# Performance work log

Hardware: AMD Instinct MI355X
Metric: run time of the kernel (lower is better)

The kernel has to match this reference:

```python
import jax, jax.numpy as jnp
import numpy as np

SHAPES = ((64, 64), (32, 32), (16, 16), (8, 8))
LEVEL_STARTS = np.concatenate([[0], np.cumsum([h * w for h, w in SHAPES])]).tolist()
N_LEVELS = 4; N_HEADS = 8; N_POINTS = 4; D_MODEL = 256; HEAD_DIM = 32; D_FFN = 1024; NUM_LAYERS = 2
LEN_IN = sum(h * w for h, w in SHAPES)
BATCH = 2


def setup_inputs():
    key = jax.random.key(0)
    ks = iter(jax.random.split(key, 40))
    r = lambda shape, s=1.0: jax.random.normal(next(ks), shape, dtype=jnp.float32) * s
    L = NUM_LAYERS
    return {
        "src": r((BATCH, LEN_IN, D_MODEL)),
        "pos": r((BATCH, LEN_IN, D_MODEL), 0.5),
        "valid_ratios": jnp.ones((BATCH, N_LEVELS, 2), jnp.float32),
        "Wv": r((L, D_MODEL, D_MODEL), 0.05), "bv": jnp.zeros((L, D_MODEL), jnp.float32),
        "Woff": r((L, D_MODEL, N_HEADS * N_LEVELS * N_POINTS * 2), 0.002),
        "boff": r((L, N_HEADS * N_LEVELS * N_POINTS * 2), 0.5),
        "Wa": r((L, D_MODEL, N_HEADS * N_LEVELS * N_POINTS), 0.05),
        "ba": jnp.zeros((L, N_HEADS * N_LEVELS * N_POINTS), jnp.float32),
        "Wo": r((L, D_MODEL, D_MODEL), 0.05), "bo": jnp.zeros((L, D_MODEL), jnp.float32),
        "g1": jnp.ones((L, D_MODEL), jnp.float32), "be1": jnp.zeros((L, D_MODEL), jnp.float32),
        "Wl1": r((L, D_MODEL, D_FFN), 0.05), "bl1": jnp.zeros((L, D_FFN), jnp.float32),
        "Wl2": r((L, D_FFN, D_MODEL), 0.05), "bl2": jnp.zeros((L, D_MODEL), jnp.float32),
        "g2": jnp.ones((L, D_MODEL), jnp.float32), "be2": jnp.zeros((L, D_MODEL), jnp.float32),
    }


def layer_norm(x, g, b, eps=1e-5):
    m = jnp.mean(x, -1, keepdims=True)
    v = jnp.mean(jnp.square(x - m), -1, keepdims=True)
    return (x - m) * jax.lax.rsqrt(v + eps) * g + b


def make_reference_points(valid_ratios):
    # DeformableTransformerEncoder.get_reference_points, vectorized per level
    refs = []
    for lvl, (H, W) in enumerate(SHAPES):
        gy, gx = jnp.meshgrid(jnp.arange(H, dtype=jnp.float32) + 0.5,
                              jnp.arange(W, dtype=jnp.float32) + 0.5, indexing="ij")
        ry = gy.reshape(-1)[None] / (valid_ratios[:, lvl, 1][:, None] * H)
        rx = gx.reshape(-1)[None] / (valid_ratios[:, lvl, 0][:, None] * W)
        refs.append(jnp.stack([rx, ry], -1))  # [N, H*W, 2]
    ref = jnp.concatenate(refs, 1)  # [N, Len, 2]
    return ref[:, :, None, :] * valid_ratios[:, None]  # [N, Len, n_levels, 2]


def ms_deform_attn(query, input_flatten, reference_points, Wv, bv, Woff, boff, Wa, ba, Wo, bo):
    N, Lq, _ = query.shape
    value = (input_flatten @ Wv + bv).reshape(N, -1, N_HEADS, HEAD_DIM)
    off = (query @ Woff + boff).reshape(N, Lq, N_HEADS, N_LEVELS, N_POINTS, 2)
    aw = (query @ Wa + ba).reshape(N, Lq, N_HEADS, N_LEVELS * N_POINTS)
    aw = jax.nn.softmax(aw, -1).reshape(N, Lq, N_HEADS, N_LEVELS, N_POINTS)
    # normalizer is (W, H) per level, as in MSDeformAttn
    normalizer = jnp.array([[w, h] for h, w in SHAPES], jnp.float32)
    loc = reference_points[:, :, None, :, None, :] + off / normalizer[None, None, None, :, None, :]
    acc = jnp.zeros((N, N_HEADS, Lq, HEAD_DIM), query.dtype)
    for lvl, (H, W) in enumerate(SHAPES):
        s = LEVEL_STARTS[lvl]
        val = value[:, s:s + H * W].transpose(0, 2, 1, 3)  # [N, heads, H*W, hd]
        # grid_sample bilinear, align_corners=False, zero padding
        x = loc[:, :, :, lvl, :, 0] * W - 0.5  # [N, Lq, heads, P]
        y = loc[:, :, :, lvl, :, 1] * H - 0.5
        x0 = jnp.floor(x); y0 = jnp.floor(y)
        wx1 = x - x0; wy1 = y - y0
        ix0 = x0.astype(jnp.int32); iy0 = y0.astype(jnp.int32)

        def corner(ix, iy, w):
            valid = (ix >= 0) & (ix < W) & (iy >= 0) & (iy < H)
            idx = jnp.clip(iy, 0, H - 1) * W + jnp.clip(ix, 0, W - 1)
            idx = idx.transpose(0, 2, 1, 3).reshape(N, N_HEADS, Lq * N_POINTS)
            g = jnp.take_along_axis(val, idx[..., None], axis=2).reshape(N, N_HEADS, Lq, N_POINTS, HEAD_DIM)
            w = jnp.where(valid, w, 0.0).transpose(0, 2, 1, 3)  # [N, heads, Lq, P]
            return g * w[..., None]

        sampled = (corner(ix0, iy0, (1 - wx1) * (1 - wy1))
                   + corner(ix0 + 1, iy0, wx1 * (1 - wy1))
                   + corner(ix0, iy0 + 1, (1 - wx1) * wy1)
                   + corner(ix0 + 1, iy0 + 1, wx1 * wy1))
        acc = acc + (sampled * aw[:, :, :, lvl].transpose(0, 2, 1, 3)[..., None]).sum(3)
    out = acc.transpose(0, 2, 1, 3).reshape(N, Lq, D_MODEL)
    return out @ Wo + bo


def reference(src, pos, valid_ratios, Wv, bv, Woff, boff, Wa, ba, Wo, bo,
              g1, be1, Wl1, bl1, Wl2, bl2, g2, be2):
    ref_pts = make_reference_points(valid_ratios)
    out = src
    for l in range(NUM_LAYERS):
        q = out + pos  # with_pos_embed
        attn = ms_deform_attn(q, out, ref_pts, Wv[l], bv[l], Woff[l], boff[l],
                              Wa[l], ba[l], Wo[l], bo[l])
        out = layer_norm(out + attn, g1[l], be1[l])
        ffn = jax.nn.relu(out @ Wl1[l] + bl1[l]) @ Wl2[l] + bl2[l]
        out = layer_norm(out + ffn, g2[l], be2[l])
    return out
```

## Files before the change

kernel.cpp:

```cpp
#include <hip/hip_runtime.h>
#include <math.h>

#define LEN   5440
#define NB    2
#define MROWS (NB * LEN)
#define DM    256
#define NH    8
#define HD    32
#define NLV   4
#define NPT   4
#define DFFN  1024

typedef __attribute__((ext_vector_type(8))) short bf16x8;
typedef __attribute__((ext_vector_type(4))) short bf16x4;
typedef __attribute__((ext_vector_type(4))) float f32x4;

__device__ __forceinline__ short f2bf(float f) {
    union { float f; unsigned u; } cv; cv.f = f;
    unsigned r = cv.u + 0x7fffu + ((cv.u >> 16) & 1u);
    return (short)(r >> 16);
}
__device__ __forceinline__ float bf2f(short s) {
    union { unsigned u; float f; } cv;
    cv.u = ((unsigned)(unsigned short)s) << 16;
    return cv.f;
}

__global__ __launch_bounds__(256) void transpose_convert_all(
    const float* __restrict__ Wv,  const float* __restrict__ Woff,
    const float* __restrict__ Wa,  const float* __restrict__ Wo,
    const float* __restrict__ Wl1, const float* __restrict__ Wl2,
    short* __restrict__ out)
{
    int bx = blockIdx.x;
    int l  = bx / 736;
    int t  = bx % 736;
    const float* src; int K, N; long doff;
    if      (t < 64)  { src = Wv;   K = 256;  N = 256;  doff = 0;      }
    else if (t < 128) { src = Woff; K = 256;  N = 256;  doff = 65536;  t -= 64;  }
    else if (t < 160) { src = Wa;   K = 256;  N = 128;  doff = 131072; t -= 128; }
    else if (t < 224) { src = Wo;   K = 256;  N = 256;  doff = 163840; t -= 160; }
    else if (t < 480) { src = Wl1;  K = 256;  N = 1024; doff = 229376; t -= 224; }
    else              { src = Wl2;  K = 1024; N = 256;  doff = 491520; t -= 480; }
    src += (long)l * K * N;
    short* dst = out + (long)l * 753664 + doff;

    const int ntx = N / 32;
    const int n0 = (t % ntx) * 32, k0 = (t / ntx) * 32;

    __shared__ short T[32][33];
    const int tid = threadIdx.x;
    {
        const int n = tid & 31, kq = tid >> 5;
        #pragma unroll
        for (int i = 0; i < 4; ++i) {
            int k = kq * 4 + i;
            T[n][k] = f2bf(src[(long)(k0 + k) * N + n0 + n]);
        }
    }
    __syncthreads();
    {
        const int k = tid & 31, nq = tid >> 5;
        #pragma unroll
        for (int i = 0; i < 4; ++i) {
            int n = nq * 4 + i;
            dst[(long)(n0 + n) * K + k0 + k] = T[n][k];
        }
    }
}

__global__ __launch_bounds__(256) void convert_src(
    const float4* __restrict__ s4, const float4* __restrict__ p4,
    bf16x4* __restrict__ curb, bf16x4* __restrict__ qb)
{
    const int i = blockIdx.x * 256 + threadIdx.x;
    float4 s = s4[i], p = p4[i];
    bf16x4 c, q;
    c[0] = f2bf(s.x); c[1] = f2bf(s.y); c[2] = f2bf(s.z); c[3] = f2bf(s.w);
    q[0] = f2bf(s.x + p.x); q[1] = f2bf(s.y + p.y);
    q[2] = f2bf(s.z + p.z); q[3] = f2bf(s.w + p.w);
    curb[i] = c; qb[i] = q;
}

template <int BN, int RELU, int OMODE>
__device__ __forceinline__ void gemm_core128(
    short* As, short* Bs,
    const short* __restrict__ A, const short* __restrict__ Wt,
    const float* __restrict__ bias, float* __restrict__ Cf,
    short* __restrict__ Cb,
    int ldc, int m0, int wrow0, int ccol0, int K)
{
    constexpr int NF = BN / 32;
    constexpr int NBJ = BN / 64;
    const int t    = threadIdx.x;
    const int wave = t >> 6, lane = t & 63;
    const int wm   = (wave & 1) * 64;
    const int wn   = (wave >> 1) * (BN / 2);
    const int lm   = lane & 15;
    const int chkg = lane >> 4;
    const int srow = t >> 2;
    const int sc   = t & 3;

    f32x4 acc[4][NF] = {};
    bf16x8 ar[2], br[NBJ];

    #pragma unroll
    for (int j = 0; j < 2; ++j)
        ar[j] = *(const bf16x8*)(A + (long)(m0 + srow + 64 * j) * K + sc * 8);
    #pragma unroll
    for (int j = 0; j < NBJ; ++j)
        br[j] = *(const bf16x8*)(Wt + (long)(wrow0 + srow + 64 * j) * K + sc * 8);

    for (int k0 = 0; k0 < K; k0 += 32) {
        __syncthreads();
        #pragma unroll
        for (int j = 0; j < 2; ++j)
            *(bf16x8*)(&As[(srow + 64 * j) * 40 + sc * 8]) = ar[j];
        #pragma unroll
        for (int j = 0; j < NBJ; ++j)
            *(bf16x8*)(&Bs[(srow + 64 * j) * 40 + sc * 8]) = br[j];
        __syncthreads();

        if (k0 + 32 < K) {
            #pragma unroll
            for (int j = 0; j < 2; ++j)
                ar[j] = *(const bf16x8*)(A + (long)(m0 + srow + 64 * j) * K + k0 + 32 + sc * 8);
            #pragma unroll
            for (int j = 0; j < NBJ; ++j)
                br[j] = *(const bf16x8*)(Wt + (long)(wrow0 + srow + 64 * j) * K + k0 + 32 + sc * 8);
        }

        bf16x8 af[4], bfv[NF];
        #pragma unroll
        for (int s = 0; s < 4; ++s)
            af[s] = *(const bf16x8*)(&As[(wm + s * 16 + lm) * 40 + chkg * 8]);
        #pragma unroll
        for (int u = 0; u < NF; ++u)
            bfv[u] = *(const bf16x8*)(&Bs[(wn + u * 16 + lm) * 40 + chkg * 8]);
        #pragma unroll
        for (int s = 0; s < 4; ++s)
            #pragma unroll
            for (int u = 0; u < NF; ++u)
                acc[s][u] = __builtin_amdgcn_mfma_f32_16x16x32_bf16(
                    af[s], bfv[u], acc[s][u], 0, 0, 0);
    }

    const int col = lane & 15;
    const int rq  = (lane >> 4) * 4;
    #pragma unroll
    for (int s = 0; s < 4; ++s) {
        #pragma unroll
        for (int u = 0; u < NF; ++u) {
            const int gn = ccol0 + wn + u * 16 + col;
            const float bb = bias[gn];
            #pragma unroll
            for (int r = 0; r < 4; ++r) {
                const int gm = m0 + wm + s * 16 + rq + r;
                float v = acc[s][u][r] + bb;
                if (RELU) v = fmaxf(v, 0.f);
                if (OMODE == 0) {
                    Cf[(long)gm * ldc + gn] = v;
                } else if (OMODE == 1) {
                    Cb[(long)gm * ldc + gn] = f2bf(v);
                } else {
                    const int n   = gm / LEN;
                    const int pix = gm - n * LEN;
                    const int h   = gn >> 5, d = gn & 31;
                    Cb[((long)(n * NH + h) * LEN + pix) * 32 + d] = f2bf(v);
                }
            }
        }
    }
}

template <int BN, int RELU, int OMODE>
__global__ __launch_bounds__(256) void gemm128(
    const short* __restrict__ A, const short* __restrict__ Wt,
    const float* __restrict__ bias, float* Cf, short* Cb, int ldc, int K)
{
    __shared__ __align__(16) short As[128 * 40];
    __shared__ __align__(16) short Bs[BN * 40];
    gemm_core128<BN, RELU, OMODE>(As, Bs, A, Wt, bias, Cf, Cb, ldc,
                                  blockIdx.y * 128, blockIdx.x * BN,
                                  blockIdx.x * BN, K);
}

__global__ __launch_bounds__(256) void gemm_qkv128(
    const short* __restrict__ curb, const short* __restrict__ qb,
    const short* __restrict__ Wt, const float* __restrict__ bv,
    const float* __restrict__ boff, const float* __restrict__ ba,
    short* __restrict__ Vb, float* __restrict__ OFF, float* __restrict__ AW)
{
    __shared__ __align__(16) short As[128 * 40];
    __shared__ __align__(16) short Bs[128 * 40];
    const int n0 = blockIdx.x * 128;
    if (n0 < 256) {
        gemm_core128<128, 0, 2>(As, Bs, curb, Wt, bv, (float*)nullptr, Vb,
                                256, blockIdx.y * 128, n0, n0, 256);
    } else if (n0 < 512) {
        gemm_core128<128, 0, 0>(As, Bs, qb, Wt, boff, OFF, (short*)nullptr,
                                256, blockIdx.y * 128, n0, n0 - 256, 256);
    } else {
        gemm_core128<128, 0, 0>(As, Bs, qb, Wt, ba, AW, (short*)nullptr,
                                128, blockIdx.y * 128, n0, n0 - 512, 256);
    }
}

__global__ __launch_bounds__(256) void gemm_ln(
    const short* __restrict__ A, const short* __restrict__ Wt,
    const float* __restrict__ bias, const float* __restrict__ resid,
    const float* __restrict__ g, const float* __restrict__ be,
    float* __restrict__ outf, short* __restrict__ outb,
    short* __restrict__ outq, const float* __restrict__ pos, int K)
{
    __shared__ __align__(16) short As[32 * 40];
    __shared__ __align__(16) short Bs[256 * 40];
    __shared__ float red[2][32][2];

    const int t    = threadIdx.x;
    const int wave = t >> 6, lane = t & 63;
    const int wm   = (wave & 1) * 16;
    const int wn   = (wave >> 1) * 128;
    const int lm   = lane & 15;
    const int chkg = lane >> 4;
    const int srow = t >> 2;
    const int sc   = t & 3;
    const int m0   = blockIdx.x * 32;
    const bool doA = (t < 128);

    f32x4 acc[8] = {};
    bf16x8 ar, br[4];

    if (doA) ar = *(const bf16x8*)(A + (long)(m0 + srow) * K + sc * 8);
    #pragma unroll
    for (int j = 0; j < 4; ++j)
        br[j] = *(const bf16x8*)(Wt + (long)(srow + 64 * j) * K + sc * 8);

    for (int k0 = 0; k0 < K; k0 += 32) {
        __syncthreads();
        if (doA) *(bf16x8*)(&As[srow * 40 + sc * 8]) = ar;
        #pragma unroll
        for (int j = 0; j < 4; ++j)
            *(bf16x8*)(&Bs[(srow + 64 * j) * 40 + sc * 8]) = br[j];
        __syncthreads();

        if (k0 + 32 < K) {
            if (doA) ar = *(const bf16x8*)(A + (long)(m0 + srow) * K + k0 + 32 + sc * 8);
            #pragma unroll
            for (int j = 0; j < 4; ++j)
                br[j] = *(const bf16x8*)(Wt + (long)(srow + 64 * j) * K + k0 + 32 + sc * 8);
        }

        bf16x8 af = *(const bf16x8*)(&As[(wm + lm) * 40 + chkg * 8]);
        #pragma unroll
        for (int u = 0; u < 8; ++u) {
            bf16x8 bfv = *(const bf16x8*)(&Bs[(wn + u * 16 + lm) * 40 + chkg * 8]);
            acc[u] = __builtin_amdgcn_mfma_f32_16x16x32_bf16(af, bfv, acc[u], 0, 0, 0);
        }
    }

    const int rq = (lane >> 4) * 4;
    #pragma unroll
    for (int u = 0; u < 8; ++u) {
        const int gn = wn + u * 16 + lm;
        const float bb = bias[gn];
        #pragma unroll
        for (int r = 0; r < 4; ++r) {
            const int gm = m0 + wm + rq + r;
            acc[u][r] += bb + resid[(long)gm * DM + gn];
        }
    }

    float rs[4], r2[4];
    #pragma unroll
    for (int r = 0; r < 4; ++r) {
        float s = 0.f, s2 = 0.f;
        #pragma unroll
        for (int u = 0; u < 8; ++u) { const float v = acc[u][r]; s += v; s2 += v * v; }
        rs[r] = s; r2[r] = s2;
    }
    #pragma unroll
    for (int o = 1; o < 16; o <<= 1) {
        #pragma unroll
        for (int r = 0; r < 4; ++r) {
            rs[r] += __shfl_xor(rs[r], o, 64);
            r2[r] += __shfl_xor(r2[r], o, 64);
        }
    }
    if (lm == 0) {
        #pragma unroll
        for (int r = 0; r < 4; ++r) {
            red[wave >> 1][wm + rq + r][0] = rs[r];
            red[wave >> 1][wm + rq + r][1] = r2[r];
        }
    }
    __syncthreads();
    #pragma unroll
    for (int r = 0; r < 4; ++r) {
        const int row = wm + rq + r;
        const float ts = red[0][row][0] + red[1][row][0];
        const float t2 = red[0][row][1] + red[1][row][1];
        const float mean = ts * (1.f / DM);
        const float var  = t2 * (1.f / DM) - mean * mean;
        rs[r] = mean;
        r2[r] = rsqrtf(var + 1e-5f);
    }
    #pragma unroll
    for (int u = 0; u < 8; ++u) {
        const int gn = wn + u * 16 + lm;
        const float gg = g[gn], bbe = be[gn];
        #pragma unroll
        for (int r = 0; r < 4; ++r) {
            const int gm = m0 + wm + rq + r;
            const float o = (acc[u][r] - rs[r]) * r2[r] * gg + bbe;
            outf[(long)gm * DM + gn] = o;
            if (outb) outb[(long)gm * DM + gn] = f2bf(o);
            if (outq) outq[(long)gm * DM + gn] = f2bf(o + pos[(long)gm * DM + gn]);
        }
    }
}

__global__ __launch_bounds__(256) void deform_attn_v3(
    const short* __restrict__ Vb,
    const float* __restrict__ OFF,
    const float* __restrict__ AW,
    const float* __restrict__ vr,
    bf16x4* __restrict__ ATTb)
{
    const int starts[5] = {0, 4096, 5120, 5376, 5440};
    const int dims[4]   = {64, 32, 16, 8};

    const int wave = threadIdx.x >> 6;
    const int lane = threadIdx.x & 63;
    const int h    = lane >> 3;
    const int d4   = lane & 7;

    const int gq = blockIdx.x * 4 + wave;
    const int n  = gq / LEN;
    const int q  = gq % LEN;

    int lq = 3;
    if (q < 4096) lq = 0; else if (q < 5120) lq = 1; else if (q < 5376) lq = 2;
    const int r  = q - starts[lq];
    const int Wq = dims[lq];
    const int gy = r / Wq, gx = r % Wq;
    const float vrxq = vr[(n * NLV + lq) * 2 + 0];
    const float vryq = vr[(n * NLV + lq) * 2 + 1];
    const float rx = (gx + 0.5f) / (vrxq * Wq);
    const float ry = (gy + 0.5f) / (vryq * Wq);

    const long row = (long)n * LEN + q;

    const float* awp = AW + row * 128 + h * 16;
    float a[16];
    float mx = -1e30f;
    #pragma unroll
    for (int i = 0; i < 16; ++i) { a[i] = awp[i]; mx = fmaxf(mx, a[i]); }
    float s = 0.f;
    #pragma unroll
    for (int i = 0; i < 16; ++i) { a[i] = __expf(a[i] - mx); s += a[i]; }
    const float inv = 1.f / s;

    const float* offp = OFF + row * 256 + h * 32;

    float4 acc = {0.f, 0.f, 0.f, 0.f};
    #pragma unroll
    for (int lvl = 0; lvl < NLV; ++lvl) {
        const int Hl = dims[lvl];
        const int Wl = Hl;
        const float fW = (float)Wl;
        const int sb = starts[lvl];
        const float lx = rx * vr[(n * NLV + lvl) * 2 + 0];
        const float ly = ry * vr[(n * NLV + lvl) * 2 + 1];
        const short* vb = Vb + ((long)(n * NH + h) * LEN + sb) * 32 + d4 * 4;
        #pragma unroll
        for (int p = 0; p < NPT; ++p) {
            const float ox = offp[lvl * 8 + p * 2 + 0];
            const float oy = offp[lvl * 8 + p * 2 + 1];
            const float x = fmaf(lx, fW, ox) - 0.5f;
            const float y = fmaf(ly, fW, oy) - 0.5f;
            const float x0f = floorf(x), y0f = floorf(y);
            const int ix0 = (int)x0f, iy0 = (int)y0f;
            const float wx1 = x - x0f, wy1 = y - y0f;
            const float wx0 = 1.f - wx1, wy0 = 1.f - wy1;

            const bool vx0 = (ix0 >= 0)     && (ix0 < Wl);
            const bool vx1 = (ix0 + 1 >= 0) && (ix0 + 1 < Wl);
            const bool vy0 = (iy0 >= 0)     && (iy0 < Hl);
            const bool vy1 = (iy0 + 1 >= 0) && (iy0 + 1 < Hl);
            const int cx0 = min(max(ix0, 0), Wl - 1);
            const int cx1 = min(max(ix0 + 1, 0), Wl - 1);
            const int cy0 = min(max(iy0, 0), Hl - 1);
            const int cy1 = min(max(iy0 + 1, 0), Hl - 1);

            const float w00 = (vx0 && vy0) ? wx0 * wy0 : 0.f;
            const float w10 = (vx1 && vy0) ? wx1 * wy0 : 0.f;
            const float w01 = (vx0 && vy1) ? wx0 * wy1 : 0.f;
            const float w11 = (vx1 && vy1) ? wx1 * wy1 : 0.f;

            const bf16x4 g00 = *(const bf16x4*)(vb + (long)(cy0 * Wl + cx0) * 32);
            const bf16x4 g10 = *(const bf16x4*)(vb + (long)(cy0 * Wl + cx1) * 32);
            const bf16x4 g01 = *(const bf16x4*)(vb + (long)(cy1 * Wl + cx0) * 32);
            const bf16x4 g11 = *(const bf16x4*)(vb + (long)(cy1 * Wl + cx1) * 32);

            const float awv = a[lvl * 4 + p] * inv;
            #pragma unroll
            for (int e = 0; e < 4; ++e) {
                float sv = w00 * bf2f(g00[e]) + w10 * bf2f(g10[e])
                         + w01 * bf2f(g01[e]) + w11 * bf2f(g11[e]);
                (&acc.x)[e] += awv * sv;
            }
        }
    }
    bf16x4 ob;
    ob[0] = f2bf(acc.x); ob[1] = f2bf(acc.y);
    ob[2] = f2bf(acc.z); ob[3] = f2bf(acc.w);
    ATTb[row * 64 + h * 8 + d4] = ob;
}

extern "C" void kernel_launch(void* const* d_in, const int* in_sizes, int n_in,
                              void* d_out, int out_size, void* d_ws, size_t ws_size,
                              hipStream_t stream)
{
    const float* src = (const float*)d_in[0];
    const float* pos = (const float*)d_in[1];
    const float* vr  = (const float*)d_in[2];
    const float* Wv_   = (const float*)d_in[3];
    const float* bv_   = (const float*)d_in[4];
    const float* Woff_ = (const float*)d_in[5];
    const float* boff_ = (const float*)d_in[6];
    const float* Wa_   = (const float*)d_in[7];
    const float* ba_   = (const float*)d_in[8];
    const float* Wo_   = (const float*)d_in[9];
    const float* bo_   = (const float*)d_in[10];
    const float* g1_   = (const float*)d_in[11];
    const float* be1_  = (const float*)d_in[12];
    const float* Wl1_  = (const float*)d_in[13];
    const float* bl1_  = (const float*)d_in[14];
    const float* Wl2_  = (const float*)d_in[15];
    const float* bl2_  = (const float*)d_in[16];
    const float* g2_   = (const float*)d_in[17];
    const float* be2_  = (const float*)d_in[18];

    const long SZ = (long)MROWS * DM;
    float* ws = (float*)d_ws;
    float* OFF  = ws;
    float* AW   = OFF + SZ;
    float* XA   = AW  + (long)MROWS * 128;
    float* XB   = XA  + SZ;
    short* Vb   = (short*)(XB + SZ);
    short* curb = Vb   + SZ;
    short* qb   = curb + SZ;
    short* ATTb = qb   + SZ;
    short* XAb  = ATTb + SZ;
    short* FFNb = XAb  + SZ;
    short* Wt   = FFNb + (long)MROWS * DFFN;

    const dim3 blk(256);
    const int GYM = MROWS / 128;
    const int GLN = MROWS / 32;

    hipLaunchKernelGGL(transpose_convert_all, dim3(1472), blk, 0, stream,
                       Wv_, Woff_, Wa_, Wo_, Wl1_, Wl2_, Wt);
    hipLaunchKernelGGL(convert_src, dim3(SZ / 4 / 256), blk, 0, stream,
                       (const float4*)src, (const float4*)pos,
                       (bf16x4*)curb, (bf16x4*)qb);

    const float* cur = src;
    for (int l = 0; l < 2; ++l) {
        const short* Wbase = Wt + (long)l * 753664;
        const float* bv   = bv_   + (long)l * DM;
        const float* boff = boff_ + (long)l * 256;
        const float* ba   = ba_   + (long)l * 128;
        const float* bo   = bo_   + (long)l * DM;
        const float* g1   = g1_   + (long)l * DM;
        const float* be1  = be1_  + (long)l * DM;
        const float* bl1  = bl1_  + (long)l * DFFN;
        const float* bl2  = bl2_  + (long)l * DM;
        const float* g2   = g2_   + (long)l * DM;
        const float* be2  = be2_  + (long)l * DM;

        hipLaunchKernelGGL(gemm_qkv128, dim3(5, GYM), blk, 0, stream,
                           curb, qb, Wbase, bv, boff, ba, Vb, OFF, AW);
        hipLaunchKernelGGL(deform_attn_v3, dim3(MROWS / 4), blk, 0, stream,
                           Vb, OFF, AW, vr, (bf16x4*)ATTb);
        hipLaunchKernelGGL(gemm_ln, dim3(GLN), blk, 0, stream,
                           ATTb, Wbase + 163840, bo, cur, g1, be1,
                           XA, XAb, (short*)nullptr, (const float*)nullptr, 256);
        hipLaunchKernelGGL((gemm128<128, 1, 1>), dim3(8, GYM), blk, 0, stream,
                           XAb, Wbase + 229376, bl1, (float*)nullptr, FFNb, 1024, 256);
        if (l == 0) {
            hipLaunchKernelGGL(gemm_ln, dim3(GLN), blk, 0, stream,
                               FFNb, Wbase + 491520, bl2, XA, g2, be2,
                               XB, curb, qb, pos, 1024);
            cur = XB;
        } else {
            hipLaunchKernelGGL(gemm_ln, dim3(GLN), blk, 0, stream,
                               FFNb, Wbase + 491520, bl2, XA, g2, be2,
                               (float*)d_out, (short*)nullptr, (short*)nullptr,
                               (const float*)nullptr, 1024);
        }
    }
}
```

Before: 315.4 us.

## Enlarge gemm_ln tile to 64 rows with K-step 64 and templated K

Reworks the fused GEMM+LayerNorm kernel so each block handles 64 rows, not 32. Each wave now covers a 64x64 output subtile with a 4x4 MFMA grid, and the K loop steps 64 per iteration instead of 32. The goal is more MFMA work per shared-memory load and per barrier, better reuse of A and B fragments, and full unrolling through the compile-time K. The cost is a grid halved to 170 blocks, which may underfill the GPU, plus higher register and LDS use per block.

```diff
diff --git a/kernel.cpp b/kernel.cpp
--- a/kernel.cpp
+++ b/kernel.cpp
@@ -206,117 +206,152 @@
     }
 }
 
+template <int K>
 __global__ __launch_bounds__(256) void gemm_ln(
     const short* __restrict__ A, const short* __restrict__ Wt,
     const float* __restrict__ bias, const float* __restrict__ resid,
     const float* __restrict__ g, const float* __restrict__ be,
     float* __restrict__ outf, short* __restrict__ outb,
-    short* __restrict__ outq, const float* __restrict__ pos, int K)
-{
-    __shared__ __align__(16) short As[32 * 40];
-    __shared__ __align__(16) short Bs[256 * 40];
-    __shared__ float red[2][32][2];
+    short* __restrict__ outq, const float* __restrict__ pos)
+{
+    __shared__ __align__(16) short As[64 * 72];
+    __shared__ __align__(16) short Bs[256 * 72];
+    __shared__ float red[4][64][2];
 
     const int t    = threadIdx.x;
     const int wave = t >> 6, lane = t & 63;
-    const int wm   = (wave & 1) * 16;
-    const int wn   = (wave >> 1) * 128;
+    const int wn   = wave * 64;
     const int lm   = lane & 15;
     const int chkg = lane >> 4;
     const int srow = t >> 2;
     const int sc   = t & 3;
-    const int m0   = blockIdx.x * 32;
-    const bool doA = (t < 128);
-
-    f32x4 acc[8] = {};
-    bf16x8 ar, br[4];
-
-    if (doA) ar = *(const bf16x8*)(A + (long)(m0 + srow) * K + sc * 8);
+    const int m0   = blockIdx.x * 64;
+
+    f32x4 acc[4][4] = {};
+    bf16x8 ar[2], br[8];
+
+    #pragma unroll
+    for (int c = 0; c < 2; ++c)
+        ar[c] = *(const bf16x8*)(A + (long)(m0 + srow) * K + c * 32 + sc * 8);
     #pragma unroll
     for (int j = 0; j < 4; ++j)
-        br[j] = *(const bf16x8*)(Wt + (long)(srow + 64 * j) * K + sc * 8);
-
-    for (int k0 = 0; k0 < K; k0 += 32) {
+        #pragma unroll
+        for (int c = 0; c < 2; ++c)
+            br[j * 2 + c] = *(const bf16x8*)(Wt + (long)(srow + 64 * j) * K + c * 32 + sc * 8);
+
+    for (int k0 = 0; k0 < K; k0 += 64) {
         __syncthreads();
-        if (doA) *(bf16x8*)(&As[srow * 40 + sc * 8]) = ar;
+        #pragma unroll
+        for (int c = 0; c < 2; ++c)
+            *(bf16x8*)(&As[srow * 72 + c * 32 + sc * 8]) = ar[c];
         #pragma unroll
         for (int j = 0; j < 4; ++j)
-            *(bf16x8*)(&Bs[(srow + 64 * j) * 40 + sc * 8]) = br[j];
+            #pragma unroll
+            for (int c = 0; c < 2; ++c)
+                *(bf16x8*)(&Bs[(srow + 64 * j) * 72 + c * 32 + sc * 8]) = br[j * 2 + c];
         __syncthreads();
 
-        if (k0 + 32 < K) {
-            if (doA) ar = *(const bf16x8*)(A + (long)(m0 + srow) * K + k0 + 32 + sc * 8);
+        if (k0 + 64 < K) {
+            #pragma unroll
+            for (int c = 0; c < 2; ++c)
+                ar[c] = *(const bf16x8*)(A + (long)(m0 + srow) * K + k0 + 64 + c * 32 + sc * 8);
             #pragma unroll
             for (int j = 0; j < 4; ++j)
-                br[j] = *(const bf16x8*)(Wt + (long)(srow + 64 * j) * K + k0 + 32 + sc * 8);
-        }
-
-        bf16x8 af = *(const bf16x8*)(&As[(wm + lm) * 40 + chkg * 8]);
-        #pragma unroll
-        for (int u = 0; u < 8; ++u) {
-            bf16x8 bfv = *(const bf16x8*)(&Bs[(wn + u * 16 + lm) * 40 + chkg * 8]);
-            acc[u] = __builtin_amdgcn_mfma_f32_16x16x32_bf16(af, bfv, acc[u], 0, 0, 0);
+                #pragma unroll
+                for (int c = 0; c < 2; ++c)
+                    br[j * 2 + c] = *(const bf16x8*)(Wt + (long)(srow + 64 * j) * K + k0 + 64 + c * 32 + sc * 8);
+        }
+
+        #pragma unroll
+        for (int kk = 0; kk < 2; ++kk) {
+            bf16x8 af[4], bfv[4];
+            #pragma unroll
+            for (int s = 0; s < 4; ++s)
+                af[s] = *(const bf16x8*)(&As[(s * 16 + lm) * 72 + kk * 32 + chkg * 8]);
+            #pragma unroll
+            for (int u = 0; u < 4; ++u)
+                bfv[u] = *(const bf16x8*)(&Bs[(wn + u * 16 + lm) * 72 + kk * 32 + chkg * 8]);
+            #pragma unroll
+            for (int s = 0; s < 4; ++s)
+                #pragma unroll
+                for (int u = 0; u < 4; ++u)
+                    acc[s][u] = __builtin_amdgcn_mfma_f32_16x16x32_bf16(
+                        af[s], bfv[u], acc[s][u], 0, 0, 0);
         }
     }
 
     const int rq = (lane >> 4) * 4;
     #pragma unroll
-    for (int u = 0; u < 8; ++u) {
+    for (int u = 0; u < 4; ++u) {
         const int gn = wn + u * 16 + lm;
         const float bb = bias[gn];
         #pragma unroll
+        for (int s = 0; s < 4; ++s)
+            #pragma unroll
+            for (int r = 0; r < 4; ++r)
+                acc[s][u][r] += bb + resid[(long)(m0 + s * 16 + rq + r) * DM + gn];
+    }
+
+    float ps[4][4], p2[4][4];
+    #pragma unroll
+    for (int s = 0; s < 4; ++s)
+        #pragma unroll
         for (int r = 0; r < 4; ++r) {
-            const int gm = m0 + wm + rq + r;
-            acc[u][r] += bb + resid[(long)gm * DM + gn];
-        }
-    }
-
-    float rs[4], r2[4];
-    #pragma unroll
-    for (int r = 0; r < 4; ++r) {
-        float s = 0.f, s2 = 0.f;
-        #pragma unroll
-        for (int u = 0; u < 8; ++u) { const float v = acc[u][r]; s += v; s2 += v * v; }
-        rs[r] = s; r2[r] = s2;
-    }
-    #pragma unroll
-    for (int o = 1; o < 16; o <<= 1) {
+            float sm = 0.f, s2 = 0.f;
+            #pragma unroll
+            for (int u = 0; u < 4; ++u) {
+                const float v = acc[s][u][r];
+                sm += v; s2 += v * v;
+            }
+            ps[s][r] = sm; p2[s][r] = s2;
+        }
+    #pragma unroll
+    for (int o = 1; o < 16; o <<= 1)
+        #pragma unroll
+        for (int s = 0; s < 4; ++s)
+            #pragma unroll
+            for (int r = 0; r < 4; ++r) {
+                ps[s][r] += __shfl_xor(ps[s][r], o, 64);
+                p2[s][r] += __shfl_xor(p2[s][r], o, 64);
+            }
+    if (lm == 0) {
+        #pragma unroll
+        for (int s = 0; s < 4; ++s)
+            #pragma unroll
+            for (int r = 0; r < 4; ++r) {
+                red[wave][s * 16 + rq + r][0] = ps[s][r];
+                red[wave][s * 16 + rq + r][1] = p2[s][r];
+            }
+    }
+    __syncthreads();
+
+    float mean[4][4], rstd[4][4];
+    #pragma unroll
+    for (int s = 0; s < 4; ++s)
         #pragma unroll
         for (int r = 0; r < 4; ++r) {
-            rs[r] += __shfl_xor(rs[r], o, 64);
-            r2[r] += __shfl_xor(r2[r], o, 64);
-        }
-    }
-    if (lm == 0) {
-        #pragma unroll
-        for (int r = 0; r < 4; ++r) {
-            red[wave >> 1][wm + rq + r][0] = rs[r];
-            red[wave >> 1][wm + rq + r][1] = r2[r];
-        }
-    }
-    __syncthreads();
-    #pragma unroll
-    for (int r = 0; r < 4; ++r) {
-        const int row = wm + rq + r;
-        const float ts = red[0][row][0] + red[1][row][0];
-        const float t2 = red[0][row][1] + red[1][row][1];
-        const float mean = ts * (1.f / DM);
-        const float var  = t2 * (1.f / DM) - mean * mean;
-        rs[r] = mean;
-        r2[r] = rsqrtf(var + 1e-5f);
-    }
-    #pragma unroll
-    for (int u = 0; u < 8; ++u) {
+            const int row = s * 16 + rq + r;
+            const float ts = red[0][row][0] + red[1][row][0] + red[2][row][0] + red[3][row][0];
+            const float t2 = red[0][row][1] + red[1][row][1] + red[2][row][1] + red[3][row][1];
+            const float m = ts * (1.f / DM);
+            mean[s][r] = m;
+            rstd[s][r] = rsqrtf(t2 * (1.f / DM) - m * m + 1e-5f);
+        }
+
+    #pragma unroll
+    for (int u = 0; u < 4; ++u) {
         const int gn = wn + u * 16 + lm;
         const float gg = g[gn], bbe = be[gn];
         #pragma unroll
-        for (int r = 0; r < 4; ++r) {
-            const int gm = m0 + wm + rq + r;
-            const float o = (acc[u][r] - rs[r]) * r2[r] * gg + bbe;
-            outf[(long)gm * DM + gn] = o;
-            if (outb) outb[(long)gm * DM + gn] = f2bf(o);
-            if (outq) outq[(long)gm * DM + gn] = f2bf(o + pos[(long)gm * DM + gn]);
-        }
+        for (int s = 0; s < 4; ++s)
+            #pragma unroll
+            for (int r = 0; r < 4; ++r) {
+                const long gm = m0 + s * 16 + rq + r;
+                const float o = (acc[s][u][r] - mean[s][r]) * rstd[s][r] * gg + bbe;
+                outf[gm * DM + gn] = o;
+                if (outb) outb[gm * DM + gn] = f2bf(o);
+                if (outq) outq[gm * DM + gn] = f2bf(o + pos[gm * DM + gn]);
+            }
     }
 }
 
@@ -458,7 +493,7 @@
 
     const dim3 blk(256);
     const int GYM = MROWS / 128;
-    const int GLN = MROWS / 32;
+    const int GLN = MROWS / 64;
 
     hipLaunchKernelGGL(transpose_convert_all, dim3(1472), blk, 0, stream,
                        Wv_, Woff_, Wa_, Wo_, Wl1_, Wl2_, Wt);
@@ -484,21 +519,21 @@
                            curb, qb, Wbase, bv, boff, ba, Vb, OFF, AW);
         hipLaunchKernelGGL(deform_attn_v3, dim3(MROWS / 4), blk, 0, stream,
                            Vb, OFF, AW, vr, (bf16x4*)ATTb);
-        hipLaunchKernelGGL(gemm_ln, dim3(GLN), blk, 0, stream,
+        hipLaunchKernelGGL((gemm_ln<256>), dim3(GLN), blk, 0, stream,
                            ATTb, Wbase + 163840, bo, cur, g1, be1,
-                           XA, XAb, (short*)nullptr, (const float*)nullptr, 256);
+                           XA, XAb, (short*)nullptr, (const float*)nullptr);
         hipLaunchKernelGGL((gemm128<128, 1, 1>), dim3(8, GYM), blk, 0, stream,
                            XAb, Wbase + 229376, bl1, (float*)nullptr, FFNb, 1024, 256);
         if (l == 0) {
-            hipLaunchKernelGGL(gemm_ln, dim3(GLN), blk, 0, stream,
+            hipLaunchKernelGGL((gemm_ln<1024>), dim3(GLN), blk, 0, stream,
                                FFNb, Wbase + 491520, bl2, XA, g2, be2,
-                               XB, curb, qb, pos, 1024);
+                               XB, curb, qb, pos);
             cur = XB;
         } else {
-            hipLaunchKernelGGL(gemm_ln, dim3(GLN), blk, 0, stream,
+            hipLaunchKernelGGL((gemm_ln<1024>), dim3(GLN), blk, 0, stream,
                                FFNb, Wbase + 491520, bl2, XA, g2, be2,
                                (float*)d_out, (short*)nullptr, (short*)nullptr,
-                               (const float*)nullptr, 1024);
-        }
-    }
-}
+                               (const float*)nullptr);
+        }
+    }
+}
```

Measured after the change: 319.9 us. No clear change (+1.5%).
